# Optimization experiments

Hardware: AMD Instinct MI355X
Metric: run time of the kernel (lower is better)

## Reference

```python
import jax, jax.numpy as jnp
import numpy as np

H = 256          # h_dim
SEQ_LEN = 10     # max history length
B = 2048         # number of queries with non-empty history
N = 327680       # total flattened neighbors across all (query, timestep) segments
NUM_SEG = B * SEQ_LEN
NUM_ENT = 20000
NUM_REL = 200


def setup_inputs() -> dict:
    key = jax.random.key(0)
    ks = jax.random.split(key, 9)
    s = jax.random.randint(ks[0], (B,), 0, NUM_ENT)
    r = jax.random.randint(ks[1], (B,), 0, NUM_REL)
    nbr_ids = jax.random.randint(ks[2], (N,), 0, NUM_ENT)
    seg_ids = jnp.sort(jax.random.randint(ks[3], (N,), 0, NUM_SEG))
    ent_embeds = jax.random.normal(ks[4], (NUM_ENT, H), dtype=jnp.float32)
    rel_embeds = jax.random.normal(ks[5], (NUM_REL, H), dtype=jnp.float32)
    W_attn = jax.random.normal(ks[6], (3 * H, H), dtype=jnp.float32) * 0.05
    b_attn = jax.random.normal(ks[7], (H,), dtype=jnp.float32) * 0.05
    v_s = jax.random.normal(ks[8], (H, 1), dtype=jnp.float32) * 0.05
    return {"s": s, "r": r, "nbr_ids": nbr_ids, "seg_ids": seg_ids,
            "ent_embeds": ent_embeds, "rel_embeds": rel_embeds,
            "W_attn": W_attn, "b_attn": b_attn, "v_s": v_s}


def reference(s, r, nbr_ids, seg_ids, ent_embeds, rel_embeds, W_attn, b_attn, v_s):
    # Per-neighbor gathers. Each neighbor belongs to segment seg = q*SEQ_LEN + t.
    q = seg_ids // SEQ_LEN                              # query index per neighbor [N]
    em = ent_embeds[nbr_ids]                            # [N, H] neighbor embeddings
    s_emb = ent_embeds[s]                               # [B, H]
    r_emb = rel_embeds[r]                               # [B, H]
    ss = s_emb[q]                                       # [N, H]
    rr = r_emb[q]                                       # [N, H]
    # Score: tanh(Linear(3H -> H)) @ v_s  -> scalar per neighbor
    x = jnp.concatenate([em, ss, rr], axis=1)           # [N, 3H]
    scores = (jnp.tanh(x @ W_attn + b_attn) @ v_s)[:, 0]  # [N]
    # Segment softmax over neighbors within each (query, timestep) segment.
    m = jax.ops.segment_max(scores, seg_ids, num_segments=NUM_SEG)  # [S]
    e = jnp.exp(scores - m[seg_ids])                    # [N]
    denom = jax.ops.segment_sum(e, seg_ids, num_segments=NUM_SEG)   # [S]
    w = e / denom[seg_ids]                              # [N]
    # Weighted sum of neighbor embeddings per segment (scatter-reduce).
    agg = jax.ops.segment_sum(w[:, None] * em, seg_ids, num_segments=NUM_SEG)  # [S, H]
    counts = jax.ops.segment_sum(jnp.ones_like(scores), seg_ids, num_segments=NUM_SEG)
    mask = (counts > 0).astype(em.dtype).reshape(B, SEQ_LEN, 1)     # present timesteps
    agg = agg.reshape(B, SEQ_LEN, H)
    ss_t = jnp.broadcast_to(s_emb[:, None, :], (B, SEQ_LEN, H))
    rr_t = jnp.broadcast_to(r_emb[:, None, :], (B, SEQ_LEN, H))
    # Padded [B, SEQ_LEN, 3H] sequence tensor (rows for empty segments are zero,
    # matching the torch code's zero-initialized padded tensor). Dropout p=0.0.
    out = jnp.concatenate([agg, ss_t, rr_t], axis=2) * mask
    return out
```

## Files before the change

### kernel.cpp

```cpp
#include <hip/hip_runtime.h>
#include <hip/hip_bf16.h>

#define H 256
#define SEQ 10
#define C2LOG2E 2.8853900817779268f
#define LOG2E 1.4426950408889634f

typedef __attribute__((ext_vector_type(8))) short bf16x8;
typedef __attribute__((ext_vector_type(4))) float f32x4;

__device__ __forceinline__ unsigned short f2bf(float x) {
    union { float f; unsigned u; } v; v.f = x;
    unsigned r = v.u + 0x7fff + ((v.u >> 16) & 1);
    return (unsigned short)(r >> 16);
}
__device__ __forceinline__ float bf2f(unsigned short b) {
    union { unsigned u; float f; } v; v.u = ((unsigned)b) << 16;
    return v.f;
}
__device__ __forceinline__ float fexp2(float x) {
    return __builtin_amdgcn_exp2f(x);
}

__global__ void prep_kernel(const float* __restrict__ W,
                            unsigned short* __restrict__ Wt,
                            const int* __restrict__ seg_ids,
                            int* __restrict__ seg_start,
                            int nWt, int n, int num_seg) {
    if ((int)blockIdx.x < nWt) {
        int idx = blockIdx.x * 256 + threadIdx.x;
        if (idx >= H * 3 * H) return;
        int nn = idx / (3 * H), k = idx % (3 * H);
        Wt[idx] = f2bf(C2LOG2E * W[k * H + nn]);
    } else {
        int j = (blockIdx.x - nWt) * 256 + threadIdx.x;
        if (j >= n) return;
        int cur = seg_ids[j];
        int prev = (j == 0) ? -1 : seg_ids[j - 1];
        for (int s2 = prev + 1; s2 <= cur; s2++) seg_start[s2] = j;
        if (j == n - 1)
            for (int s2 = cur + 1; s2 <= num_seg; s2++) seg_start[s2] = n;
    }
}

__global__ void gemm_bf16_kernel(const float* __restrict__ entf,
                                 const int* __restrict__ sidx,
                                 const int* __restrict__ ridx,
                                 const float* __restrict__ rel,
                                 const unsigned short* __restrict__ Wt,
                                 const float* __restrict__ bias,
                                 unsigned short* __restrict__ comb,
                                 float* __restrict__ Eq,
                                 int nEntBlk, int M0, int M1) {
    __shared__ unsigned short As[64][40];
    bool isEnt = (int)blockIdx.x < nEntBlk;
    int m0 = (isEnt ? blockIdx.x : (blockIdx.x - nEntBlk)) * 64;
    int M = isEnt ? M0 : M1;
    int K = isEnt ? H : 2 * H;
    int k0 = isEnt ? 0 : H;

    int t = threadIdx.x;
    int sr = t >> 2;
    int sc = (t & 3) * 8;
    int wave = t >> 6, lane = t & 63;
    int lr = lane & 15, lg = lane >> 4;

    f32x4 acc[4][4];
#pragma unroll
    for (int i = 0; i < 4; i++)
#pragma unroll
        for (int jn = 0; jn < 4; jn++) acc[i][jn] = (f32x4){0.f, 0.f, 0.f, 0.f};

    const unsigned short* bp[4];
#pragma unroll
    for (int bn = 0; bn < 4; bn++)
        bp[bn] = Wt + (size_t)(wave * 64 + bn * 16 + lr) * (3 * H) + k0 + lg * 8;

    for (int kk = 0; kk < K; kk += 32) {
        bf16x8 av = {};
        int gm = m0 + sr;
        if (gm < M) {
            const float* src;
            if (isEnt) {
                src = entf + (size_t)gm * H + kk + sc;
            } else {
                int k = kk + sc;
                src = (k < H) ? (entf + (size_t)sidx[gm] * H + k)
                              : (rel + (size_t)ridx[gm] * H + (k - H));
            }
            float4 f0 = *reinterpret_cast<const float4*>(src);
            float4 f1 = *reinterpret_cast<const float4*>(src + 4);
            av[0] = (short)f2bf(f0.x); av[1] = (short)f2bf(f0.y);
            av[2] = (short)f2bf(f0.z); av[3] = (short)f2bf(f0.w);
            av[4] = (short)f2bf(f1.x); av[5] = (short)f2bf(f1.y);
            av[6] = (short)f2bf(f1.z); av[7] = (short)f2bf(f1.w);
            if (isEnt)
                *reinterpret_cast<bf16x8*>(comb + (size_t)gm * 512 + 256 + kk + sc) = av;
        }
        *reinterpret_cast<bf16x8*>(&As[sr][sc]) = av;

        bf16x8 bfr[4];
#pragma unroll
        for (int bn = 0; bn < 4; bn++)
            bfr[bn] = *reinterpret_cast<const bf16x8*>(bp[bn] + kk);

        __syncthreads();
        bf16x8 afr[4];
#pragma unroll
        for (int am = 0; am < 4; am++)
            afr[am] = *reinterpret_cast<const bf16x8*>(&As[am * 16 + lr][lg * 8]);
#pragma unroll
        for (int am = 0; am < 4; am++)
#pragma unroll
            for (int bn = 0; bn < 4; bn++)
                acc[am][bn] = __builtin_amdgcn_mfma_f32_16x16x32_bf16(
                    afr[am], bfr[bn], acc[am][bn], 0, 0, 0);
        __syncthreads();
    }

#pragma unroll
    for (int bn = 0; bn < 4; bn++) {
        int col = wave * 64 + bn * 16 + lr;
        float bv = isEnt ? 0.f : C2LOG2E * bias[col];
#pragma unroll
        for (int am = 0; am < 4; am++) {
#pragma unroll
            for (int rr = 0; rr < 4; rr++) {
                int row = m0 + am * 16 + lg * 4 + rr;
                if (row < M) {
                    float ex = fexp2(acc[am][bn][rr] + bv);
                    if (isEnt)
                        comb[(size_t)row * 512 + col] = f2bf(ex);
                    else
                        Eq[(size_t)row * H + col] = ex;
                }
            }
        }
    }
}

__global__ void __launch_bounds__(128)
fused_agg_kernel(const int* __restrict__ nbr_ids,
                 const int* __restrict__ seg_start,
                 const unsigned short* __restrict__ comb,
                 const float* __restrict__ Eq,
                 const float* __restrict__ v_s,
                 const float* __restrict__ ent_embeds,
                 const float* __restrict__ rel_embeds,
                 const int* __restrict__ s,
                 const int* __restrict__ r,
                 float* __restrict__ out, int num_seg) {
    int seg = blockIdx.x * 2 + (threadIdx.x >> 6);
    if (seg >= num_seg) return;
    int lane = threadIdx.x & 63;
    int g = lane >> 4, li = lane & 15;
    int cb = li * 16;
    int c4 = lane * 4;
    int b = seg / SEQ;
    int start = seg_start[seg], end = seg_start[seg + 1];
    float* orow = out + (size_t)seg * (3 * H);

    if (start == end) {
        float4 z = {0.f, 0.f, 0.f, 0.f};
        *reinterpret_cast<float4*>(orow + c4) = z;
        *reinterpret_cast<float4*>(orow + H + c4) = z;
        *reinterpret_cast<float4*>(orow + 2 * H + c4) = z;
        return;
    }

    float4 ssv = *reinterpret_cast<const float4*>(ent_embeds + (size_t)s[b] * H + c4);
    float4 rrv = *reinterpret_cast<const float4*>(rel_embeds + (size_t)r[b] * H + c4);

    float vm2[16];
    float vsum = 0.f;
    {
        const float4* vp = reinterpret_cast<const float4*>(v_s + cb);
#pragma unroll
        for (int k = 0; k < 4; k++) {
            float4 tv = vp[k];
            vm2[4 * k + 0] = -2.f * LOG2E * tv.x; vm2[4 * k + 1] = -2.f * LOG2E * tv.y;
            vm2[4 * k + 2] = -2.f * LOG2E * tv.z; vm2[4 * k + 3] = -2.f * LOG2E * tv.w;
            vsum += LOG2E * (tv.x + tv.y + tv.z + tv.w);
        }
    }

    float qv[16];
    {
        const float4* qp = reinterpret_cast<const float4*>(Eq + (size_t)b * H + cb);
#pragma unroll
        for (int k = 0; k < 4; k++) {
            float4 tq = qp[k];
            qv[4 * k + 0] = tq.x; qv[4 * k + 1] = tq.y;
            qv[4 * k + 2] = tq.z; qv[4 * k + 3] = tq.w;
        }
    }

    float acc[16];
#pragma unroll
    for (int k = 0; k < 16; k++) acc[k] = 0.f;
    float lpart = 0.f;

    int cc = end - start;
    int nitm = (cc + 3) >> 2;

    bf16x8 bp0[3], bp1[3], be0[3], be1[3];
#pragma unroll
    for (int u = 0; u < 3; u++) { bp0[u] = {}; bp1[u] = {}; be0[u] = {}; be1[u] = {}; }
#pragma unroll
    for (int u = 0; u < 3; u++) {
        int j = 4 * u + g;
        if (j < cc) {
            const unsigned short* row = comb + (size_t)nbr_ids[start + j] * 512 + cb;
            bp0[u] = *reinterpret_cast<const bf16x8*>(row);
            bp1[u] = *reinterpret_cast<const bf16x8*>(row + 8);
            be0[u] = *reinterpret_cast<const bf16x8*>(row + 256);
            be1[u] = *reinterpret_cast<const bf16x8*>(row + 264);
        }
    }

    for (int ji = 0; ji < nitm; ji += 3) {
#pragma unroll
        for (int u = 0; u < 3; u++) {
            float sa = 0.f, sb = 0.f;
#pragma unroll
            for (int k = 0; k < 8; k += 2) {
                float a0 = fmaf(bf2f((unsigned short)bp0[u][k]), qv[k], 1.f);
                float a1 = fmaf(bf2f((unsigned short)bp1[u][k]), qv[8 + k], 1.f);
                float num = vm2[k] * a1;
                num = fmaf(vm2[8 + k], a0, num);
                sa = fmaf(num, __builtin_amdgcn_rcpf(a0 * a1), sa);
                float b0 = fmaf(bf2f((unsigned short)bp0[u][k + 1]), qv[k + 1], 1.f);
                float b1 = fmaf(bf2f((unsigned short)bp1[u][k + 1]), qv[9 + k], 1.f);
                float numb = vm2[k + 1] * b1;
                numb = fmaf(vm2[9 + k], b0, numb);
                sb = fmaf(numb, __builtin_amdgcn_rcpf(b0 * b1), sb);
            }
            float s16 = sa + sb + vsum;
            s16 += __shfl_xor(s16, 1);
            s16 += __shfl_xor(s16, 2);
            s16 += __shfl_xor(s16, 4);
            s16 += __shfl_xor(s16, 8);
            float e = fexp2(s16);
            e = (4 * (ji + u) + g < cc) ? e : 0.f;
            lpart += e;
#pragma unroll
            for (int k = 0; k < 8; k++) {
                acc[k] = fmaf(e, bf2f((unsigned short)be0[u][k]), acc[k]);
                acc[8 + k] = fmaf(e, bf2f((unsigned short)be1[u][k]), acc[8 + k]);
            }
            int jn = 4 * (ji + u + 3) + g;
            if (jn < cc) {
                const unsigned short* rown = comb + (size_t)nbr_ids[start + jn] * 512 + cb;
                bp0[u] = *reinterpret_cast<const bf16x8*>(rown);
                bp1[u] = *reinterpret_cast<const bf16x8*>(rown + 8);
                be0[u] = *reinterpret_cast<const bf16x8*>(rown + 256);
                be1[u] = *reinterpret_cast<const bf16x8*>(rown + 264);
            }
        }
    }

    lpart += __shfl_xor(lpart, 16);
    lpart += __shfl_xor(lpart, 32);
    float invl = 1.f / lpart;

    int gb0 = g & 1, gb1 = g >> 1;
    float t1[8];
#pragma unroll
    for (int j = 0; j < 8; j++) {
        int sl0 = (j < 4) ? j : 4 + j;
        int sl1 = sl0 + 4;
        float mine = gb0 ? acc[sl1] : acc[sl0];
        float opp  = gb0 ? acc[sl0] : acc[sl1];
        t1[j] = mine + __shfl_xor(opp, 16);
    }
    float4 o;
#pragma unroll
    for (int j = 0; j < 4; j++) {
        float mine = gb1 ? t1[4 + j] : t1[j];
        float opp  = gb1 ? t1[j] : t1[4 + j];
        float fin = (mine + __shfl_xor(opp, 32)) * invl;
        if (j == 0) o.x = fin;
        else if (j == 1) o.y = fin;
        else if (j == 2) o.z = fin;
        else o.w = fin;
    }
    *reinterpret_cast<float4*>(orow + cb + 4 * g) = o;
    *reinterpret_cast<float4*>(orow + H + c4) = ssv;
    *reinterpret_cast<float4*>(orow + 2 * H + c4) = rrv;
}

extern "C" void kernel_launch(void* const* d_in, const int* in_sizes, int n_in,
                              void* d_out, int out_size, void* d_ws, size_t ws_size,
                              hipStream_t stream) {
    const int* s = (const int*)d_in[0];
    const int* r = (const int*)d_in[1];
    const int* nbr_ids = (const int*)d_in[2];
    const int* seg_ids = (const int*)d_in[3];
    const float* ent_embeds = (const float*)d_in[4];
    const float* rel_embeds = (const float*)d_in[5];
    const float* W_attn = (const float*)d_in[6];
    const float* b_attn = (const float*)d_in[7];
    const float* v_s = (const float*)d_in[8];
    float* out = (float*)d_out;

    int B = in_sizes[0];
    int N = in_sizes[2];
    int num_ent = in_sizes[4] / H;
    int num_seg = B * SEQ;

    char* ws = (char*)d_ws;
    unsigned short* comb = (unsigned short*)ws;
    unsigned short* Wt = comb + (size_t)num_ent * 512;
    float* Eq = (float*)(Wt + (size_t)H * 3 * H);
    int* seg_start = (int*)(Eq + (size_t)B * H);

    int nWt = (H * 3 * H + 255) / 256;
    int nSeg = (N + 255) / 256;
    prep_kernel<<<nWt + nSeg, 256, 0, stream>>>(W_attn, Wt, seg_ids, seg_start,
                                                nWt, N, num_seg);

    int nEntBlk = (num_ent + 63) / 64;
    int nQBlk = B / 64;
    gemm_bf16_kernel<<<nEntBlk + nQBlk, 256, 0, stream>>>(
        ent_embeds, s, r, rel_embeds, Wt, b_attn, comb, Eq,
        nEntBlk, num_ent, B);

    fused_agg_kernel<<<(num_seg + 1) / 2, 128, 0, stream>>>(
        nbr_ids, seg_start, comb, Eq, v_s,
        ent_embeds, rel_embeds, s, r, out, num_seg);
}
```

Measured before the change: 103.1 us.

## Use packed f32x2 math, single-step prefetch and setprio in neighbor loop

Rewrites the per-neighbor inner loop to unpack bf16 pairs with shifts and masks and compute them with packed two-wide FMAs (which can map to packed FP32 instructions). The three-deep register prefetch ring is replaced with a simpler one-ahead prefetch of the next neighbor's row. The compute section is bracketed with s_setprio to favour issue of math over other waves. The intent is fewer ALU instructions and less register pressure, at the cost of a shallower prefetch that may expose more gather latency.

```diff
diff --git a/kernel.cpp b/kernel.cpp
--- a/kernel.cpp
+++ b/kernel.cpp
@@ -8,6 +8,7 @@
 
 typedef __attribute__((ext_vector_type(8))) short bf16x8;
 typedef __attribute__((ext_vector_type(4))) float f32x4;
+typedef __attribute__((ext_vector_type(2))) float f32x2;
 
 __device__ __forceinline__ unsigned short f2bf(float x) {
     union { float f; unsigned u; } v; v.f = x;
@@ -20,6 +21,13 @@
 }
 __device__ __forceinline__ float fexp2(float x) {
     return __builtin_amdgcn_exp2f(x);
+}
+__device__ __forceinline__ f32x2 up2(unsigned u) {
+    union { unsigned u32; float f; } lo, hi;
+    lo.u32 = u << 16;
+    hi.u32 = u & 0xffff0000u;
+    f32x2 r; r.x = lo.f; r.y = hi.f;
+    return r;
 }
 
 __global__ void prep_kernel(const float* __restrict__ W,
@@ -184,84 +192,94 @@
         }
     }
 
-    float qv[16];
+    f32x2 qv2[8];
     {
         const float4* qp = reinterpret_cast<const float4*>(Eq + (size_t)b * H + cb);
 #pragma unroll
         for (int k = 0; k < 4; k++) {
             float4 tq = qp[k];
-            qv[4 * k + 0] = tq.x; qv[4 * k + 1] = tq.y;
-            qv[4 * k + 2] = tq.z; qv[4 * k + 3] = tq.w;
-        }
-    }
-
-    float acc[16];
-#pragma unroll
-    for (int k = 0; k < 16; k++) acc[k] = 0.f;
+            qv2[2 * k + 0] = (f32x2){tq.x, tq.y};
+            qv2[2 * k + 1] = (f32x2){tq.z, tq.w};
+        }
+    }
+
+    f32x2 acc2[8];
+#pragma unroll
+    for (int k = 0; k < 8; k++) acc2[k] = (f32x2){0.f, 0.f};
     float lpart = 0.f;
 
     int cc = end - start;
     int nitm = (cc + 3) >> 2;
 
-    bf16x8 bp0[3], bp1[3], be0[3], be1[3];
-#pragma unroll
-    for (int u = 0; u < 3; u++) { bp0[u] = {}; bp1[u] = {}; be0[u] = {}; be1[u] = {}; }
-#pragma unroll
-    for (int u = 0; u < 3; u++) {
-        int j = 4 * u + g;
-        if (j < cc) {
-            const unsigned short* row = comb + (size_t)nbr_ids[start + j] * 512 + cb;
-            bp0[u] = *reinterpret_cast<const bf16x8*>(row);
-            bp1[u] = *reinterpret_cast<const bf16x8*>(row + 8);
-            be0[u] = *reinterpret_cast<const bf16x8*>(row + 256);
-            be1[u] = *reinterpret_cast<const bf16x8*>(row + 264);
-        }
-    }
-
-    for (int ji = 0; ji < nitm; ji += 3) {
-#pragma unroll
-        for (int u = 0; u < 3; u++) {
-            float sa = 0.f, sb = 0.f;
-#pragma unroll
-            for (int k = 0; k < 8; k += 2) {
-                float a0 = fmaf(bf2f((unsigned short)bp0[u][k]), qv[k], 1.f);
-                float a1 = fmaf(bf2f((unsigned short)bp1[u][k]), qv[8 + k], 1.f);
-                float num = vm2[k] * a1;
-                num = fmaf(vm2[8 + k], a0, num);
-                sa = fmaf(num, __builtin_amdgcn_rcpf(a0 * a1), sa);
-                float b0 = fmaf(bf2f((unsigned short)bp0[u][k + 1]), qv[k + 1], 1.f);
-                float b1 = fmaf(bf2f((unsigned short)bp1[u][k + 1]), qv[9 + k], 1.f);
-                float numb = vm2[k + 1] * b1;
-                numb = fmaf(vm2[9 + k], b0, numb);
-                sb = fmaf(numb, __builtin_amdgcn_rcpf(b0 * b1), sb);
-            }
-            float s16 = sa + sb + vsum;
-            s16 += __shfl_xor(s16, 1);
-            s16 += __shfl_xor(s16, 2);
-            s16 += __shfl_xor(s16, 4);
-            s16 += __shfl_xor(s16, 8);
-            float e = fexp2(s16);
-            e = (4 * (ji + u) + g < cc) ? e : 0.f;
-            lpart += e;
-#pragma unroll
-            for (int k = 0; k < 8; k++) {
-                acc[k] = fmaf(e, bf2f((unsigned short)be0[u][k]), acc[k]);
-                acc[8 + k] = fmaf(e, bf2f((unsigned short)be1[u][k]), acc[8 + k]);
-            }
-            int jn = 4 * (ji + u + 3) + g;
-            if (jn < cc) {
-                const unsigned short* rown = comb + (size_t)nbr_ids[start + jn] * 512 + cb;
-                bp0[u] = *reinterpret_cast<const bf16x8*>(rown);
-                bp1[u] = *reinterpret_cast<const bf16x8*>(rown + 8);
-                be0[u] = *reinterpret_cast<const bf16x8*>(rown + 256);
-                be1[u] = *reinterpret_cast<const bf16x8*>(rown + 264);
-            }
-        }
+    uint4 p0 = {}, p1 = {}, e0 = {}, e1 = {};
+    if (g < cc) {
+        const unsigned short* row = comb + (size_t)nbr_ids[start + g] * 512 + cb;
+        p0 = *reinterpret_cast<const uint4*>(row);
+        p1 = *reinterpret_cast<const uint4*>(row + 8);
+        e0 = *reinterpret_cast<const uint4*>(row + 256);
+        e1 = *reinterpret_cast<const uint4*>(row + 264);
+    }
+
+    const f32x2 one2 = (f32x2){1.f, 1.f};
+
+    for (int ji = 0; ji < nitm; ji++) {
+        uint4 p0n = {}, p1n = {}, e0n = {}, e1n = {};
+        int jn = 4 * (ji + 1) + g;
+        if (jn < cc) {
+            const unsigned short* rown = comb + (size_t)nbr_ids[start + jn] * 512 + cb;
+            p0n = *reinterpret_cast<const uint4*>(rown);
+            p1n = *reinterpret_cast<const uint4*>(rown + 8);
+            e0n = *reinterpret_cast<const uint4*>(rown + 256);
+            e1n = *reinterpret_cast<const uint4*>(rown + 264);
+        }
+
+        __builtin_amdgcn_s_setprio(1);
+        float sa = 0.f, sb = 0.f;
+#define PAIR(comp, qj, vlo, vhi, dst)                                      \
+        {                                                                  \
+            f32x2 a = __builtin_elementwise_fma(up2(comp), qv2[qj], one2); \
+            float num = vlo * a.y;                                         \
+            num = fmaf(vhi, a.x, num);                                     \
+            dst = fmaf(num, __builtin_amdgcn_rcpf(a.x * a.y), dst);        \
+        }
+        PAIR(p0.x, 0, vm2[0],  vm2[1],  sa)
+        PAIR(p0.y, 1, vm2[2],  vm2[3],  sb)
+        PAIR(p0.z, 2, vm2[4],  vm2[5],  sa)
+        PAIR(p0.w, 3, vm2[6],  vm2[7],  sb)
+        PAIR(p1.x, 4, vm2[8],  vm2[9],  sa)
+        PAIR(p1.y, 5, vm2[10], vm2[11], sb)
+        PAIR(p1.z, 6, vm2[12], vm2[13], sa)
+        PAIR(p1.w, 7, vm2[14], vm2[15], sb)
+#undef PAIR
+        float s16 = sa + sb + vsum;
+        s16 += __shfl_xor(s16, 1);
+        s16 += __shfl_xor(s16, 2);
+        s16 += __shfl_xor(s16, 4);
+        s16 += __shfl_xor(s16, 8);
+        float e = fexp2(s16);
+        e = (4 * ji + g < cc) ? e : 0.f;
+        lpart += e;
+        f32x2 e2; e2.x = e; e2.y = e;
+        acc2[0] = __builtin_elementwise_fma(e2, up2(e0.x), acc2[0]);
+        acc2[1] = __builtin_elementwise_fma(e2, up2(e0.y), acc2[1]);
+        acc2[2] = __builtin_elementwise_fma(e2, up2(e0.z), acc2[2]);
+        acc2[3] = __builtin_elementwise_fma(e2, up2(e0.w), acc2[3]);
+        acc2[4] = __builtin_elementwise_fma(e2, up2(e1.x), acc2[4]);
+        acc2[5] = __builtin_elementwise_fma(e2, up2(e1.y), acc2[5]);
+        acc2[6] = __builtin_elementwise_fma(e2, up2(e1.z), acc2[6]);
+        acc2[7] = __builtin_elementwise_fma(e2, up2(e1.w), acc2[7]);
+        __builtin_amdgcn_s_setprio(0);
+
+        p0 = p0n; p1 = p1n; e0 = e0n; e1 = e1n;
     }
 
     lpart += __shfl_xor(lpart, 16);
     lpart += __shfl_xor(lpart, 32);
     float invl = 1.f / lpart;
+
+    float acc[16];
+#pragma unroll
+    for (int j = 0; j < 8; j++) { acc[2 * j] = acc2[j].x; acc[2 * j + 1] = acc2[j].y; }
 
     int gb0 = g & 1, gb1 = g >> 1;
     float t1[8];
```

Result: faster. 99.38 us (-3.6%).
